# Performance work log

Hardware: AMD Instinct MI355X
Metric: run time of the kernel (lower is better)

Reference implementation:

```python
import jax, jax.numpy as jnp
import numpy as np

B, T, C = 2, 2048, 2048
H = 16
D = C // H  # head_dim = 128


def rotate_half(x):
    x1, x2 = jnp.split(x, 2, axis=-1)
    return jnp.concatenate([-x2, x1], axis=-1)


def apply_rotary(q, k, cos, sin):
    # q,k: (B,H,T,D); cos,sin: (T,D/2)
    cos2 = jnp.concatenate([cos, cos], axis=-1)[None, None]  # (1,1,T,D)
    sin2 = jnp.concatenate([sin, sin], axis=-1)[None, None]
    return q * cos2 + rotate_half(q) * sin2, k * cos2 + rotate_half(k) * sin2


def setup_inputs() -> dict:
    key = jax.random.key(0)
    k1, k2, k3, k4 = jax.random.split(key, 4)
    x = jax.random.normal(k1, (B, T, C), dtype=jnp.float32)
    w_qkv = jax.random.normal(k2, (C, 3 * C), dtype=jnp.float32) * (C ** -0.5)
    w_out = jax.random.normal(k3, (C, C), dtype=jnp.float32) * (C ** -0.5)
    pos = jnp.arange(T, dtype=jnp.float32)[:, None]
    inv_freq = 1.0 / (10000.0 ** (jnp.arange(0, D, 2, dtype=jnp.float32) / D))  # (D/2,)
    ang = pos * inv_freq[None, :]  # (T, D/2)
    return {"x": x, "w_qkv": w_qkv, "w_out": w_out,
            "cos": jnp.cos(ang), "sin": jnp.sin(ang)}


def reference(x, w_qkv, w_out, cos, sin):
    b, t, c = x.shape
    qkv = x @ w_qkv  # (B,T,3C)
    qkv = qkv.reshape(b, t, 3, H, D)
    q, k, v = qkv[:, :, 0], qkv[:, :, 1], qkv[:, :, 2]  # (B,T,H,D)
    q = q.transpose(0, 2, 1, 3)  # (B,H,T,D)
    k = k.transpose(0, 2, 1, 3)
    v = v.transpose(0, 2, 1, 3)
    q, k = apply_rotary(q, k, cos, sin)
    scale = 1.0 / jnp.sqrt(jnp.asarray(D, dtype=x.dtype))
    scores = jnp.einsum('bhqd,bhkd->bhqk', q, k) * scale  # (B,H,T,T)
    causal = jnp.tril(jnp.ones((t, t), dtype=bool))
    scores = jnp.where(causal[None, None], scores, jnp.asarray(-jnp.inf, dtype=scores.dtype))
    attn = jax.nn.softmax(scores, axis=-1)
    out = jnp.einsum('bhqk,bhkd->bhqd', attn, v)  # (B,H,T,D)
    out = out.transpose(0, 2, 1, 3).reshape(b, t, c)
    return out @ w_out
```

## Files before the change

kernel.cpp:

```cpp
#include <hip/hip_runtime.h>


typedef __attribute__((ext_vector_type(8))) short short8;
typedef __attribute__((ext_vector_type(4))) float floatx4;
typedef __attribute__((ext_vector_type(4))) unsigned int uint4v;

#define MFMA16(a, b, c) __builtin_amdgcn_mfma_f32_16x16x32_bf16(a, b, c, 0, 0, 0)

__device__ inline unsigned short f2bf(float f) {
    union { float f; unsigned int i; } v; v.f = f;
    unsigned int r = v.i + 0x7fff + ((v.i >> 16) & 1);
    return (unsigned short)(r >> 16);
}

__device__ inline void gl2lds16(const unsigned short* g, unsigned short* l) {
    __builtin_amdgcn_global_load_lds(
        (const __attribute__((address_space(1))) unsigned int*)g,
        (__attribute__((address_space(3))) unsigned int*)l, 16, 0, 0);
}

__global__ __launch_bounds__(256) void cvt_k(const float* __restrict__ in,
                                             unsigned short* __restrict__ out, int n) {
    int i = (blockIdx.x * 256 + threadIdx.x) * 8;
    if (i + 7 < n) {
        float4 v0 = *(const float4*)(&in[i]);
        float4 v1 = *(const float4*)(&in[i + 4]);
        ushort4 o0, o1;
        o0.x = f2bf(v0.x); o0.y = f2bf(v0.y); o0.z = f2bf(v0.z); o0.w = f2bf(v0.w);
        o1.x = f2bf(v1.x); o1.y = f2bf(v1.y); o1.z = f2bf(v1.z); o1.w = f2bf(v1.w);
        *(ushort4*)(&out[i])     = o0;
        *(ushort4*)(&out[i + 4]) = o1;
    } else {
        for (int j = i; j < n; j++) out[j] = f2bf(in[j]);
    }
}

__global__ __launch_bounds__(256) void transpose_f2b_k(const float* __restrict__ in,
                                                       unsigned short* __restrict__ out,
                                                       int R, int Cc) {
    __shared__ unsigned short tile[32][33];
    int ct = blockIdx.x * 32;
    int rt = blockIdx.y * 32;
    int tx = threadIdx.x & 31;
    int ty = threadIdx.x >> 5;
#pragma unroll
    for (int i = 0; i < 32; i += 8)
        tile[ty + i][tx] = f2bf(in[(size_t)(rt + ty + i) * Cc + ct + tx]);
    __syncthreads();
#pragma unroll
    for (int i = 0; i < 32; i += 8)
        out[(size_t)(ct + ty + i) * R + rt + tx] = tile[tx][ty + i];
}

__global__ __launch_bounds__(256) void transpose_v_k(const unsigned short* __restrict__ qkv,
                                                     unsigned short* __restrict__ VT) {
    __shared__ unsigned short tile[32][33];
    int t0 = blockIdx.x * 32;
    int d0 = blockIdx.y * 32;
    int bh = blockIdx.z;
    int b = bh >> 4, h = bh & 15;
    int tx = threadIdx.x & 31;
    int ty = threadIdx.x >> 5;
#pragma unroll
    for (int i = 0; i < 32; i += 8)
        tile[ty + i][tx] =
            qkv[((size_t)(b * 2048 + t0 + ty + i) * 3 + 2) * 2048 + h * 128 + d0 + tx];
    __syncthreads();
#pragma unroll
    for (int i = 0; i < 32; i += 8)
        VT[((size_t)bh * 128 + d0 + ty + i) * 2048 + t0 + tx] = tile[tx][ty + i];
}

__global__ __launch_bounds__(256) void rotary_k(unsigned short* qkv,
                                                const float* __restrict__ cosT,
                                                const float* __restrict__ sinT) {
    int idx = blockIdx.x * 256 + threadIdx.x;
    int d    = idx & 63;
    int h    = (idx >> 6) & 15;
    int part = (idx >> 10) & 1;
    int t    = (idx >> 11) & 2047;
    int b    = idx >> 22;
    size_t base = ((size_t)(b * 2048 + t) * 3 + part) * 2048 + h * 128;
    float c = cosT[t * 64 + d];
    float s = sinT[t * 64 + d];
    union { unsigned int i; float f; } u1, u2;
    u1.i = ((unsigned int)qkv[base + d]) << 16;
    u2.i = ((unsigned int)qkv[base + d + 64]) << 16;
    float x1 = u1.f, x2 = u2.f;
    qkv[base + d]      = f2bf(x1 * c - x2 * s);
    qkv[base + d + 64] = f2bf(x2 * c + x1 * s);
}

template <bool OUTF32>
__global__ __launch_bounds__(256) void gemm_bt(const unsigned short* __restrict__ A, long lda,
                                               const unsigned short* __restrict__ Bt,
                                               void* __restrict__ Co, long ldc,
                                               int M, int N, int K) {
    __shared__ unsigned short a_lds[128 * 32];
    __shared__ unsigned short b_lds[128 * 32];
    int m0 = blockIdx.y * 128, n0 = blockIdx.x * 128;
    int tid = threadIdx.x;
    int lane = tid & 63, w = tid >> 6;
    int wm = (w >> 1) * 64, wn = (w & 1) * 64;
    int lr = lane & 15, quad = lane >> 4, lk = quad * 8;

    floatx4 acc[4][4];
    floatx4 zero4 = {0.f, 0.f, 0.f, 0.f};
#pragma unroll
    for (int i = 0; i < 4; i++)
#pragma unroll
        for (int j = 0; j < 4; j++) acc[i][j] = zero4;

    for (int k0 = 0; k0 < K; k0 += 32) {
#pragma unroll
        for (int i = 0; i < 2; i++) {
            int c = w * 128 + i * 64 + lane;
            int row = c >> 2, seg = (c & 3) * 8;
            gl2lds16(&A[(size_t)(m0 + row) * lda + k0 + seg], &a_lds[c * 8]);
            gl2lds16(&Bt[(size_t)(n0 + row) * K + k0 + seg], &b_lds[c * 8]);
        }
        __syncthreads();
        short8 af[4], bfr[4];
#pragma unroll
        for (int i = 0; i < 4; i++)
            af[i] = *(const short8*)(&a_lds[(wm + i * 16 + lr) * 32 + lk]);
#pragma unroll
        for (int j = 0; j < 4; j++)
            bfr[j] = *(const short8*)(&b_lds[(wn + j * 16 + lr) * 32 + lk]);
#pragma unroll
        for (int i = 0; i < 4; i++)
#pragma unroll
            for (int j = 0; j < 4; j++)
                acc[i][j] = MFMA16(af[i], bfr[j], acc[i][j]);
        __syncthreads();
    }
#pragma unroll
    for (int i = 0; i < 4; i++)
#pragma unroll
        for (int j = 0; j < 4; j++)
#pragma unroll
            for (int r = 0; r < 4; r++) {
                int row = m0 + wm + i * 16 + quad * 4 + r;
                int col = n0 + wn + j * 16 + lr;
                if (OUTF32)
                    ((float*)Co)[(size_t)row * ldc + col] = acc[i][j][r];
                else
                    ((unsigned short*)Co)[(size_t)row * ldc + col] = f2bf(acc[i][j][r]);
            }
}

__global__ __launch_bounds__(512) void attn_fast(unsigned short* qkv,
                                                 const unsigned short* __restrict__ VT) {
    const int T = 2048, Cc = 2048, Dd = 128;
    int qt = 15 - (int)blockIdx.x;
    int bh = blockIdx.y;
    int b = bh >> 4, h = bh & 15;
    int tid = threadIdx.x, lane = tid & 63, w = tid >> 6;
    int lr = lane & 15, quad = lane >> 4, lk = quad * 8;
    int t0 = qt * 128;

    __shared__ __align__(16) unsigned short k_lds[64][136];
    __shared__ __align__(16) unsigned short vT_lds[128][72];
    __shared__ __align__(16) unsigned short p_lds[8][16][72];

    short8 qf[4];
    {
        size_t qrow = (size_t)(b * T + t0 + w * 16 + lr) * 3 * Cc + h * Dd;
#pragma unroll
        for (int c = 0; c < 4; c++)
            qf[c] = *(const short8*)(&qkv[qrow + c * 32 + lk]);
    }

    floatx4 o_acc[8];
    floatx4 zero4 = {0.f, 0.f, 0.f, 0.f};
#pragma unroll
    for (int i = 0; i < 8; i++) o_acc[i] = zero4;
    float m_i[4], l_i[4];
#pragma unroll
    for (int r = 0; r < 4; r++) { m_i[r] = -1e30f; l_i[r] = 0.f; }

    const float scale = 0.08838834764831845f;
    int nkt = 2 * qt + 2;

    for (int kt = 0; kt < nkt; kt++) {
        int tk0 = kt * 64;
#pragma unroll
        for (int i = 0; i < 2; i++) {
            int c = tid + i * 512;
            int row = c >> 4;
            int c8 = (c & 15) * 8;
            *(uint4v*)(&k_lds[row][c8]) =
                *(const uint4v*)(&qkv[((size_t)(b * T + tk0 + row) * 3 + 1) * Cc + h * Dd + c8]);
        }
#pragma unroll
        for (int i = 0; i < 2; i++) {
            int c = tid + i * 512;
            int dd = c >> 3;
            int kk = (c & 7) * 8;
            *(uint4v*)(&vT_lds[dd][kk]) =
                *(const uint4v*)(&VT[((size_t)bh * Dd + dd) * T + tk0 + kk]);
        }
        __syncthreads();

        if (tk0 <= t0 + w * 16 + 15) {
            floatx4 s[4];
#pragma unroll
            for (int n = 0; n < 4; n++) {
                s[n] = zero4;
#pragma unroll
                for (int c = 0; c < 4; c++) {
                    short8 kb = *(const short8*)(&k_lds[n * 16 + lr][c * 32 + lk]);
                    s[n] = MFMA16(qf[c], kb, s[n]);
                }
            }

            float rmax[4];
#pragma unroll
            for (int r = 0; r < 4; r++) {
                int tqr = t0 + w * 16 + quad * 4 + r;
                float mx = -1e30f;
#pragma unroll
                for (int n = 0; n < 4; n++) {
                    int tk = tk0 + n * 16 + lr;
                    float sv = s[n][r] * scale;
                    sv = (tk > tqr) ? -1e30f : sv;
                    s[n][r] = sv;
                    mx = fmaxf(mx, sv);
                }
                rmax[r] = mx;
            }
#pragma unroll
            for (int off = 1; off < 16; off <<= 1)
#pragma unroll
                for (int r = 0; r < 4; r++)
                    rmax[r] = fmaxf(rmax[r], __shfl_xor(rmax[r], off, 64));

            float alpha[4], rsum[4];
#pragma unroll
            for (int r = 0; r < 4; r++) {
                float mn = fmaxf(m_i[r], rmax[r]);
                alpha[r] = __expf(m_i[r] - mn);
                m_i[r] = mn;
                rsum[r] = 0.f;
            }
#pragma unroll
            for (int n = 0; n < 4; n++)
#pragma unroll
                for (int r = 0; r < 4; r++) {
                    float p = __expf(s[n][r] - m_i[r]);
                    rsum[r] += p;
                    p_lds[w][quad * 4 + r][n * 16 + lr] = f2bf(p);
                }
#pragma unroll
            for (int off = 1; off < 16; off <<= 1)
#pragma unroll
                for (int r = 0; r < 4; r++)
                    rsum[r] += __shfl_xor(rsum[r], off, 64);
#pragma unroll
            for (int r = 0; r < 4; r++) l_i[r] = l_i[r] * alpha[r] + rsum[r];

#pragma unroll
            for (int dt = 0; dt < 8; dt++)
#pragma unroll
                for (int r = 0; r < 4; r++) o_acc[dt][r] *= alpha[r];

            short8 pa[2];
#pragma unroll
            for (int kc = 0; kc < 2; kc++)
                pa[kc] = *(const short8*)(&p_lds[w][lr][kc * 32 + lk]);
#pragma unroll
            for (int dt = 0; dt < 8; dt++) {
#pragma unroll
                for (int kc = 0; kc < 2; kc++) {
                    short8 vb = *(const short8*)(&vT_lds[dt * 16 + lr][kc * 32 + lk]);
                    o_acc[dt] = MFMA16(pa[kc], vb, o_acc[dt]);
                }
            }
        }
        __syncthreads();
    }

#pragma unroll
    for (int dt = 0; dt < 8; dt++)
#pragma unroll
        for (int r = 0; r < 4; r++) {
            int row = t0 + w * 16 + quad * 4 + r;
            int col = dt * 16 + lr;
            qkv[(size_t)(b * T + row) * 3 * Cc + h * Dd + col] = f2bf(o_acc[dt][r] * (1.0f / l_i[r]));
        }
}

extern "C" void kernel_launch(void* const* d_in, const int* in_sizes, int n_in,
                              void* d_out, int out_size, void* d_ws, size_t ws_size,
                              hipStream_t stream) {
    const float* x    = (const float*)d_in[0];
    const float* wqkv = (const float*)d_in[1];
    const float* wout = (const float*)d_in[2];
    const float* cosT = (const float*)d_in[3];
    const float* sinT = (const float*)d_in[4];
    float* out = (float*)d_out;

    unsigned short* qkv = (unsigned short*)d_ws;
    const size_t QKV = 25165824, XBF = 8388608;
    unsigned short* xbf = qkv + QKV;
    unsigned short* wTq = xbf + XBF;
    unsigned short* VT  = xbf;
    unsigned short* wTo = wTq;

    cvt_k<<<4096, 256, 0, stream>>>(x, xbf, 8388608);
    transpose_f2b_k<<<dim3(192, 64), 256, 0, stream>>>(wqkv, wTq, 2048, 6144);
    gemm_bt<false><<<dim3(48, 32), 256, 0, stream>>>(xbf, 2048, wTq, qkv, 6144,
                                                     4096, 6144, 2048);
    rotary_k<<<32768, 256, 0, stream>>>(qkv, cosT, sinT);
    transpose_f2b_k<<<dim3(64, 64), 256, 0, stream>>>(wout, wTo, 2048, 2048);
    transpose_v_k<<<dim3(64, 4, 32), 256, 0, stream>>>(qkv, VT);
    attn_fast<<<dim3(16, 32), 512, 0, stream>>>(qkv, VT);
    gemm_bt<true><<<dim3(16, 32), 256, 0, stream>>>(qkv, 6144, wTo, out, 2048,
                                                    4096, 2048, 2048);
}
```

Measured before the change: 495.9 us.

## Pair causal query tiles per block with double-buffered async K/V staging

The attention kernel now gives each 256-thread block two 64-row query tiles, one early and one late (lo and 31-lo), so causal work is balanced across blocks. K and V tiles are loaded straight into LDS with global_load_lds into two buffers, so the next tile loads while the current one is computed. LDS layouts switch from padded rows to XOR-swizzled rows to avoid bank conflicts, and launch bounds allow two blocks per CU. In exchange, each thread keeps two sets of accumulators, which raises register pressure.

```diff
diff --git a/kernel.cpp b/kernel.cpp
--- a/kernel.cpp
+++ b/kernel.cpp
@@ -149,144 +149,177 @@
             }
 }
 
-__global__ __launch_bounds__(512) void attn_fast(unsigned short* qkv,
-                                                 const unsigned short* __restrict__ VT) {
+__device__ __forceinline__ void attn_core(const short8 (&qf)[4], floatx4 (&o_acc)[8],
+                                          float (&m_i)[4], float (&l_i)[4],
+                                          const unsigned short* __restrict__ kb_lds,
+                                          const unsigned short* __restrict__ vb_lds,
+                                          unsigned short* __restrict__ p_w,
+                                          int qrow0, int tk0, int lr, int quad) {
+    floatx4 zero4 = {0.f, 0.f, 0.f, 0.f};
+    const float scale = 0.08838834764831845f;
+
+    floatx4 s[4];
+#pragma unroll
+    for (int n = 0; n < 4; n++) {
+        s[n] = zero4;
+        int key = n * 16 + lr;
+#pragma unroll
+        for (int c = 0; c < 4; c++) {
+            short8 kb = *(const short8*)(&kb_lds[key * 128 + (((c * 4 + quad) ^ (key & 7)) * 8)]);
+            s[n] = MFMA16(qf[c], kb, s[n]);
+        }
+    }
+
+    float rmax[4];
+#pragma unroll
+    for (int r = 0; r < 4; r++) {
+        int tqr = qrow0 + quad * 4 + r;
+        float mx = -1e30f;
+#pragma unroll
+        for (int n = 0; n < 4; n++) {
+            int tk = tk0 + n * 16 + lr;
+            float sv = s[n][r] * scale;
+            sv = (tk > tqr) ? -1e30f : sv;
+            s[n][r] = sv;
+            mx = fmaxf(mx, sv);
+        }
+        rmax[r] = mx;
+    }
+#pragma unroll
+    for (int off = 1; off < 16; off <<= 1)
+#pragma unroll
+        for (int r = 0; r < 4; r++)
+            rmax[r] = fmaxf(rmax[r], __shfl_xor(rmax[r], off, 64));
+
+    float alpha[4], rsum[4];
+#pragma unroll
+    for (int r = 0; r < 4; r++) {
+        float mn = fmaxf(m_i[r], rmax[r]);
+        alpha[r] = __expf(m_i[r] - mn);
+        m_i[r] = mn;
+        rsum[r] = 0.f;
+    }
+#pragma unroll
+    for (int n = 0; n < 4; n++)
+#pragma unroll
+        for (int r = 0; r < 4; r++) {
+            float p = __expf(s[n][r] - m_i[r]);
+            rsum[r] += p;
+            int q = quad * 4 + r;
+            p_w[q * 64 + (((n * 2 + (lr >> 3)) ^ (q & 7)) * 8) + (lr & 7)] = f2bf(p);
+        }
+#pragma unroll
+    for (int off = 1; off < 16; off <<= 1)
+#pragma unroll
+        for (int r = 0; r < 4; r++)
+            rsum[r] += __shfl_xor(rsum[r], off, 64);
+#pragma unroll
+    for (int r = 0; r < 4; r++) l_i[r] = l_i[r] * alpha[r] + rsum[r];
+
+#pragma unroll
+    for (int dt = 0; dt < 8; dt++)
+#pragma unroll
+        for (int r = 0; r < 4; r++) o_acc[dt][r] *= alpha[r];
+
+    short8 pa[2];
+#pragma unroll
+    for (int kc = 0; kc < 2; kc++)
+        pa[kc] = *(const short8*)(&p_w[lr * 64 + (((kc * 4 + quad) ^ (lr & 7)) * 8)]);
+#pragma unroll
+    for (int dt = 0; dt < 8; dt++) {
+        int d = dt * 16 + lr;
+#pragma unroll
+        for (int kc = 0; kc < 2; kc++) {
+            short8 vb = *(const short8*)(&vb_lds[d * 64 + (((kc * 4 + quad) ^ (d & 7)) * 8)]);
+            o_acc[dt] = MFMA16(pa[kc], vb, o_acc[dt]);
+        }
+    }
+}
+
+__global__ __launch_bounds__(256, 2) void attn_fast(unsigned short* qkv,
+                                                    const unsigned short* __restrict__ VT) {
     const int T = 2048, Cc = 2048, Dd = 128;
-    int qt = 15 - (int)blockIdx.x;
+    int a = blockIdx.x;
+    int hi = 31 - a, lo = a;
     int bh = blockIdx.y;
     int b = bh >> 4, h = bh & 15;
     int tid = threadIdx.x, lane = tid & 63, w = tid >> 6;
     int lr = lane & 15, quad = lane >> 4, lk = quad * 8;
-    int t0 = qt * 128;
-
-    __shared__ __align__(16) unsigned short k_lds[64][136];
-    __shared__ __align__(16) unsigned short vT_lds[128][72];
-    __shared__ __align__(16) unsigned short p_lds[8][16][72];
-
-    short8 qf[4];
+    int t0_hi = hi * 64, t0_lo = lo * 64;
+
+    __shared__ __align__(16) unsigned short k_lds[2][64 * 128];
+    __shared__ __align__(16) unsigned short v_lds[2][128 * 64];
+    __shared__ __align__(16) unsigned short p_lds[4][16 * 64];
+
+    short8 qf_hi[4], qf_lo[4];
     {
-        size_t qrow = (size_t)(b * T + t0 + w * 16 + lr) * 3 * Cc + h * Dd;
-#pragma unroll
-        for (int c = 0; c < 4; c++)
-            qf[c] = *(const short8*)(&qkv[qrow + c * 32 + lk]);
-    }
-
-    floatx4 o_acc[8];
+        size_t qr_hi = (size_t)(b * T + t0_hi + w * 16 + lr) * 3 * Cc + h * Dd;
+        size_t qr_lo = (size_t)(b * T + t0_lo + w * 16 + lr) * 3 * Cc + h * Dd;
+#pragma unroll
+        for (int c = 0; c < 4; c++) {
+            qf_hi[c] = *(const short8*)(&qkv[qr_hi + c * 32 + lk]);
+            qf_lo[c] = *(const short8*)(&qkv[qr_lo + c * 32 + lk]);
+        }
+    }
+
+    floatx4 o_hi[8], o_lo[8];
     floatx4 zero4 = {0.f, 0.f, 0.f, 0.f};
 #pragma unroll
-    for (int i = 0; i < 8; i++) o_acc[i] = zero4;
-    float m_i[4], l_i[4];
-#pragma unroll
-    for (int r = 0; r < 4; r++) { m_i[r] = -1e30f; l_i[r] = 0.f; }
-
-    const float scale = 0.08838834764831845f;
-    int nkt = 2 * qt + 2;
-
+    for (int i = 0; i < 8; i++) { o_hi[i] = zero4; o_lo[i] = zero4; }
+    float m_hi[4], l_hi[4], m_lo[4], l_lo[4];
+#pragma unroll
+    for (int r = 0; r < 4; r++) {
+        m_hi[r] = -1e30f; l_hi[r] = 0.f;
+        m_lo[r] = -1e30f; l_lo[r] = 0.f;
+    }
+
+    auto stage = [&](int buf, int kt) {
+        int tk0 = kt * 64;
+#pragma unroll
+        for (int i = 0; i < 4; i++) {
+            int c = i * 256 + tid;
+            int key = c >> 4, sp = c & 15;
+            int slot = sp ^ (key & 7);
+            gl2lds16(&qkv[((size_t)(b * T + tk0 + key) * 3 + 1) * Cc + h * Dd + slot * 8],
+                     &k_lds[buf][c * 8]);
+        }
+#pragma unroll
+        for (int i = 0; i < 4; i++) {
+            int c = i * 256 + tid;
+            int d = c >> 3, sp = c & 7;
+            int slot = sp ^ (d & 7);
+            gl2lds16(&VT[((size_t)bh * Dd + d) * T + tk0 + slot * 8],
+                     &v_lds[buf][c * 8]);
+        }
+    };
+
+    int nkt = hi + 1;
+    stage(0, 0);
+    __syncthreads();
+    int cur = 0;
     for (int kt = 0; kt < nkt; kt++) {
+        if (kt + 1 < nkt) stage(cur ^ 1, kt + 1);
         int tk0 = kt * 64;
-#pragma unroll
-        for (int i = 0; i < 2; i++) {
-            int c = tid + i * 512;
-            int row = c >> 4;
-            int c8 = (c & 15) * 8;
-            *(uint4v*)(&k_lds[row][c8]) =
-                *(const uint4v*)(&qkv[((size_t)(b * T + tk0 + row) * 3 + 1) * Cc + h * Dd + c8]);
-        }
-#pragma unroll
-        for (int i = 0; i < 2; i++) {
-            int c = tid + i * 512;
-            int dd = c >> 3;
-            int kk = (c & 7) * 8;
-            *(uint4v*)(&vT_lds[dd][kk]) =
-                *(const uint4v*)(&VT[((size_t)bh * Dd + dd) * T + tk0 + kk]);
-        }
+        attn_core(qf_hi, o_hi, m_hi, l_hi, k_lds[cur], v_lds[cur], p_lds[w],
+                  t0_hi + w * 16, tk0, lr, quad);
+        if (kt <= lo)
+            attn_core(qf_lo, o_lo, m_lo, l_lo, k_lds[cur], v_lds[cur], p_lds[w],
+                      t0_lo + w * 16, tk0, lr, quad);
         __syncthreads();
-
-        if (tk0 <= t0 + w * 16 + 15) {
-            floatx4 s[4];
-#pragma unroll
-            for (int n = 0; n < 4; n++) {
-                s[n] = zero4;
-#pragma unroll
-                for (int c = 0; c < 4; c++) {
-                    short8 kb = *(const short8*)(&k_lds[n * 16 + lr][c * 32 + lk]);
-                    s[n] = MFMA16(qf[c], kb, s[n]);
-                }
-            }
-
-            float rmax[4];
-#pragma unroll
-            for (int r = 0; r < 4; r++) {
-                int tqr = t0 + w * 16 + quad * 4 + r;
-                float mx = -1e30f;
-#pragma unroll
-                for (int n = 0; n < 4; n++) {
-                    int tk = tk0 + n * 16 + lr;
-                    float sv = s[n][r] * scale;
-                    sv = (tk > tqr) ? -1e30f : sv;
-                    s[n][r] = sv;
-                    mx = fmaxf(mx, sv);
-                }
-                rmax[r] = mx;
-            }
-#pragma unroll
-            for (int off = 1; off < 16; off <<= 1)
-#pragma unroll
-                for (int r = 0; r < 4; r++)
-                    rmax[r] = fmaxf(rmax[r], __shfl_xor(rmax[r], off, 64));
-
-            float alpha[4], rsum[4];
-#pragma unroll
-            for (int r = 0; r < 4; r++) {
-                float mn = fmaxf(m_i[r], rmax[r]);
-                alpha[r] = __expf(m_i[r] - mn);
-                m_i[r] = mn;
-                rsum[r] = 0.f;
-            }
-#pragma unroll
-            for (int n = 0; n < 4; n++)
-#pragma unroll
-                for (int r = 0; r < 4; r++) {
-                    float p = __expf(s[n][r] - m_i[r]);
-                    rsum[r] += p;
-                    p_lds[w][quad * 4 + r][n * 16 + lr] = f2bf(p);
-                }
-#pragma unroll
-            for (int off = 1; off < 16; off <<= 1)
-#pragma unroll
-                for (int r = 0; r < 4; r++)
-                    rsum[r] += __shfl_xor(rsum[r], off, 64);
-#pragma unroll
-            for (int r = 0; r < 4; r++) l_i[r] = l_i[r] * alpha[r] + rsum[r];
-
-#pragma unroll
-            for (int dt = 0; dt < 8; dt++)
-#pragma unroll
-                for (int r = 0; r < 4; r++) o_acc[dt][r] *= alpha[r];
-
-            short8 pa[2];
-#pragma unroll
-            for (int kc = 0; kc < 2; kc++)
-                pa[kc] = *(const short8*)(&p_lds[w][lr][kc * 32 + lk]);
-#pragma unroll
-            for (int dt = 0; dt < 8; dt++) {
-#pragma unroll
-                for (int kc = 0; kc < 2; kc++) {
-                    short8 vb = *(const short8*)(&vT_lds[dt * 16 + lr][kc * 32 + lk]);
-                    o_acc[dt] = MFMA16(pa[kc], vb, o_acc[dt]);
-                }
-            }
-        }
-        __syncthreads();
+        cur ^= 1;
     }
 
 #pragma unroll
     for (int dt = 0; dt < 8; dt++)
 #pragma unroll
         for (int r = 0; r < 4; r++) {
-            int row = t0 + w * 16 + quad * 4 + r;
             int col = dt * 16 + lr;
-            qkv[(size_t)(b * T + row) * 3 * Cc + h * Dd + col] = f2bf(o_acc[dt][r] * (1.0f / l_i[r]));
+            int row_h = t0_hi + w * 16 + quad * 4 + r;
+            qkv[(size_t)(b * T + row_h) * 3 * Cc + h * Dd + col] =
+                f2bf(o_hi[dt][r] * (1.0f / l_hi[r]));
+            int row_l = t0_lo + w * 16 + quad * 4 + r;
+            qkv[(size_t)(b * T + row_l) * 3 * Cc + h * Dd + col] =
+                f2bf(o_lo[dt][r] * (1.0f / l_lo[r]));
         }
 }
 
@@ -314,7 +347,7 @@
     rotary_k<<<32768, 256, 0, stream>>>(qkv, cosT, sinT);
     transpose_f2b_k<<<dim3(64, 64), 256, 0, stream>>>(wout, wTo, 2048, 2048);
     transpose_v_k<<<dim3(64, 4, 32), 256, 0, stream>>>(qkv, VT);
-    attn_fast<<<dim3(16, 32), 512, 0, stream>>>(qkv, VT);
+    attn_fast<<<dim3(16, 32), 256, 0, stream>>>(qkv, VT);
     gemm_bt<true><<<dim3(16, 32), 256, 0, stream>>>(qkv, 6144, wTo, out, 2048,
                                                     4096, 2048, 2048);
 }
```

Measured after the change: 648.0 us. +30.7%, slower.

## Prefetch next K/V tile into registers and XOR-swizzle attention LDS layout

Applied to the files above, without the earlier changes.

The attention kernel now loads the next K and V^T tile from global memory into registers while the current tile is being computed, so global latency overlaps with the MFMA work. The registers are written to LDS at the start of the next iteration. The K and V LDS buffers drop their padding in favour of an XOR-swizzled layout to avoid bank conflicts, and the launch bounds now request 4 blocks per CU. This costs extra registers for the staged tiles and may reduce occupancy or cause spills under the tighter launch bound.

```diff
diff --git a/kernel.cpp b/kernel.cpp
--- a/kernel.cpp
+++ b/kernel.cpp
@@ -149,8 +149,94 @@
             }
 }
 
-__global__ __launch_bounds__(512) void attn_fast(unsigned short* qkv,
-                                                 const unsigned short* __restrict__ VT) {
+__device__ __forceinline__ void attn_core(const short8 (&qf)[4], floatx4 (&o_acc)[8],
+                                          float (&m_i)[4], float (&l_i)[4],
+                                          const unsigned short* kb_lds,
+                                          const unsigned short* vb_lds,
+                                          unsigned short* p_w,
+                                          int qrow0, int tk0, int lr, int quad, int lk) {
+    floatx4 zero4 = {0.f, 0.f, 0.f, 0.f};
+    const float scale = 0.08838834764831845f;
+
+    floatx4 s[4];
+#pragma unroll
+    for (int n = 0; n < 4; n++) {
+        s[n] = zero4;
+#pragma unroll
+        for (int c = 0; c < 4; c++) {
+            short8 kb = *(const short8*)(
+                &kb_lds[(n * 16 + lr) * 128 + (((c * 4 + quad) ^ lr) * 8)]);
+            s[n] = MFMA16(qf[c], kb, s[n]);
+        }
+    }
+
+    float rmax[4];
+#pragma unroll
+    for (int r = 0; r < 4; r++) {
+        int tqr = qrow0 + quad * 4 + r;
+        float mx = -1e30f;
+#pragma unroll
+        for (int n = 0; n < 4; n++) {
+            int tk = tk0 + n * 16 + lr;
+            float sv = s[n][r] * scale;
+            sv = (tk > tqr) ? -1e30f : sv;
+            s[n][r] = sv;
+            mx = fmaxf(mx, sv);
+        }
+        rmax[r] = mx;
+    }
+#pragma unroll
+    for (int off = 1; off < 16; off <<= 1)
+#pragma unroll
+        for (int r = 0; r < 4; r++)
+            rmax[r] = fmaxf(rmax[r], __shfl_xor(rmax[r], off, 64));
+
+    float alpha[4], rsum[4];
+#pragma unroll
+    for (int r = 0; r < 4; r++) {
+        float mn = fmaxf(m_i[r], rmax[r]);
+        alpha[r] = __expf(m_i[r] - mn);
+        m_i[r] = mn;
+        rsum[r] = 0.f;
+    }
+#pragma unroll
+    for (int n = 0; n < 4; n++)
+#pragma unroll
+        for (int r = 0; r < 4; r++) {
+            float p = __expf(s[n][r] - m_i[r]);
+            rsum[r] += p;
+            p_w[(quad * 4 + r) * 72 + n * 16 + lr] = f2bf(p);
+        }
+#pragma unroll
+    for (int off = 1; off < 16; off <<= 1)
+#pragma unroll
+        for (int r = 0; r < 4; r++)
+            rsum[r] += __shfl_xor(rsum[r], off, 64);
+#pragma unroll
+    for (int r = 0; r < 4; r++) l_i[r] = l_i[r] * alpha[r] + rsum[r];
+
+#pragma unroll
+    for (int dt = 0; dt < 8; dt++)
+#pragma unroll
+        for (int r = 0; r < 4; r++) o_acc[dt][r] *= alpha[r];
+
+    short8 pa[2];
+#pragma unroll
+    for (int kc = 0; kc < 2; kc++)
+        pa[kc] = *(const short8*)(&p_w[lr * 72 + kc * 32 + lk]);
+#pragma unroll
+    for (int dt = 0; dt < 8; dt++) {
+#pragma unroll
+        for (int kc = 0; kc < 2; kc++) {
+            short8 vb = *(const short8*)(
+                &vb_lds[(dt * 16 + lr) * 64 + (((kc * 4 + quad) ^ (lr & 7)) * 8)]);
+            o_acc[dt] = MFMA16(pa[kc], vb, o_acc[dt]);
+        }
+    }
+}
+
+__global__ __launch_bounds__(512, 4) void attn_fast(unsigned short* qkv,
+                                                    const unsigned short* __restrict__ VT) {
     const int T = 2048, Cc = 2048, Dd = 128;
     int qt = 15 - (int)blockIdx.x;
     int bh = blockIdx.y;
@@ -159,8 +245,8 @@
     int lr = lane & 15, quad = lane >> 4, lk = quad * 8;
     int t0 = qt * 128;
 
-    __shared__ __align__(16) unsigned short k_lds[64][136];
-    __shared__ __align__(16) unsigned short vT_lds[128][72];
+    __shared__ __align__(16) unsigned short k_lds[64 * 128];
+    __shared__ __align__(16) unsigned short v_lds[128 * 64];
     __shared__ __align__(16) unsigned short p_lds[8][16][72];
 
     short8 qf[4];
@@ -179,104 +265,43 @@
 #pragma unroll
     for (int r = 0; r < 4; r++) { m_i[r] = -1e30f; l_i[r] = 0.f; }
 
-    const float scale = 0.08838834764831845f;
+    int krow[2], kslot[2], vrow[2], vslot[2];
+#pragma unroll
+    for (int i = 0; i < 2; i++) {
+        int c = i * 512 + tid;
+        krow[i] = c >> 4; kslot[i] = c & 15;
+        vrow[i] = c >> 3; vslot[i] = c & 7;
+    }
+    uint4v kA[2], vA[2];
+    auto gload = [&](int kt) {
+        int tk0 = kt * 64;
+#pragma unroll
+        for (int i = 0; i < 2; i++) {
+            kA[i] = *(const uint4v*)(
+                &qkv[((size_t)(b * T + tk0 + krow[i]) * 3 + 1) * Cc + h * Dd + kslot[i] * 8]);
+            vA[i] = *(const uint4v*)(
+                &VT[((size_t)bh * Dd + vrow[i]) * T + tk0 + vslot[i] * 8]);
+        }
+    };
+    auto lwrite = [&]() {
+#pragma unroll
+        for (int i = 0; i < 2; i++) {
+            *(uint4v*)(&k_lds[krow[i] * 128 + ((kslot[i] ^ (krow[i] & 15)) * 8)]) = kA[i];
+            *(uint4v*)(&v_lds[vrow[i] * 64 + ((vslot[i] ^ (vrow[i] & 7)) * 8)]) = vA[i];
+        }
+    };
+
     int nkt = 2 * qt + 2;
+    gload(0);
 
     for (int kt = 0; kt < nkt; kt++) {
+        lwrite();
+        __syncthreads();
+        if (kt + 1 < nkt) gload(kt + 1);
         int tk0 = kt * 64;
-#pragma unroll
-        for (int i = 0; i < 2; i++) {
-            int c = tid + i * 512;
-            int row = c >> 4;
-            int c8 = (c & 15) * 8;
-            *(uint4v*)(&k_lds[row][c8]) =
-                *(const uint4v*)(&qkv[((size_t)(b * T + tk0 + row) * 3 + 1) * Cc + h * Dd + c8]);
-        }
-#pragma unroll
-        for (int i = 0; i < 2; i++) {
-            int c = tid + i * 512;
-            int dd = c >> 3;
-            int kk = (c & 7) * 8;
-            *(uint4v*)(&vT_lds[dd][kk]) =
-                *(const uint4v*)(&VT[((size_t)bh * Dd + dd) * T + tk0 + kk]);
-        }
-        __syncthreads();
-
-        if (tk0 <= t0 + w * 16 + 15) {
-            floatx4 s[4];
-#pragma unroll
-            for (int n = 0; n < 4; n++) {
-                s[n] = zero4;
-#pragma unroll
-                for (int c = 0; c < 4; c++) {
-                    short8 kb = *(const short8*)(&k_lds[n * 16 + lr][c * 32 + lk]);
-                    s[n] = MFMA16(qf[c], kb, s[n]);
-                }
-            }
-
-            float rmax[4];
-#pragma unroll
-            for (int r = 0; r < 4; r++) {
-                int tqr = t0 + w * 16 + quad * 4 + r;
-                float mx = -1e30f;
-#pragma unroll
-                for (int n = 0; n < 4; n++) {
-                    int tk = tk0 + n * 16 + lr;
-                    float sv = s[n][r] * scale;
-                    sv = (tk > tqr) ? -1e30f : sv;
-                    s[n][r] = sv;
-                    mx = fmaxf(mx, sv);
-                }
-                rmax[r] = mx;
-            }
-#pragma unroll
-            for (int off = 1; off < 16; off <<= 1)
-#pragma unroll
-                for (int r = 0; r < 4; r++)
-                    rmax[r] = fmaxf(rmax[r], __shfl_xor(rmax[r], off, 64));
-
-            float alpha[4], rsum[4];
-#pragma unroll
-            for (int r = 0; r < 4; r++) {
-                float mn = fmaxf(m_i[r], rmax[r]);
-                alpha[r] = __expf(m_i[r] - mn);
-                m_i[r] = mn;
-                rsum[r] = 0.f;
-            }
-#pragma unroll
-            for (int n = 0; n < 4; n++)
-#pragma unroll
-                for (int r = 0; r < 4; r++) {
-                    float p = __expf(s[n][r] - m_i[r]);
-                    rsum[r] += p;
-                    p_lds[w][quad * 4 + r][n * 16 + lr] = f2bf(p);
-                }
-#pragma unroll
-            for (int off = 1; off < 16; off <<= 1)
-#pragma unroll
-                for (int r = 0; r < 4; r++)
-                    rsum[r] += __shfl_xor(rsum[r], off, 64);
-#pragma unroll
-            for (int r = 0; r < 4; r++) l_i[r] = l_i[r] * alpha[r] + rsum[r];
-
-#pragma unroll
-            for (int dt = 0; dt < 8; dt++)
-#pragma unroll
-                for (int r = 0; r < 4; r++) o_acc[dt][r] *= alpha[r];
-
-            short8 pa[2];
-#pragma unroll
-            for (int kc = 0; kc < 2; kc++)
-                pa[kc] = *(const short8*)(&p_lds[w][lr][kc * 32 + lk]);
-#pragma unroll
-            for (int dt = 0; dt < 8; dt++) {
-#pragma unroll
-                for (int kc = 0; kc < 2; kc++) {
-                    short8 vb = *(const short8*)(&vT_lds[dt * 16 + lr][kc * 32 + lk]);
-                    o_acc[dt] = MFMA16(pa[kc], vb, o_acc[dt]);
-                }
-            }
-        }
+        if (tk0 <= t0 + w * 16 + 15)
+            attn_core(qf, o_acc, m_i, l_i, k_lds, v_lds, &p_lds[w][0][0],
+                      t0 + w * 16, tk0, lr, quad, lk);
         __syncthreads();
     }
 
```

Measured after the change: 502.8 us. Within noise of the previous version (+1.4%).
